# Optimization experiments

Hardware: AMD Instinct MI355X
Metric: run time of the kernel (lower is better)

## Reference

```python
import jax, jax.numpy as jnp
import numpy as np

MARGIN = 0.3
MIN_POS_DIST = 0.1
PUSH_SCALE = 2.0
DISSIMILAR_REL = 1  # dissimilar_relation_ids == {1}


def setup_inputs() -> dict:
    key = jax.random.key(0)
    k1, k2, k3, k4, k5 = jax.random.split(key, 5)
    B, D = 16384, 1024
    h = jax.random.normal(k1, (B, D), dtype=jnp.float32)
    t = jax.random.normal(k2, (B, D), dtype=jnp.float32)
    r = jax.random.normal(k3, (B, D), dtype=jnp.float32)
    relation_ids = jax.random.randint(k4, (B,), 0, 10, dtype=jnp.int64 if jax.config.jax_enable_x64 else jnp.int32)
    neg = jax.random.randint(k5, (B,), 0, B, dtype=relation_ids.dtype)
    idx = jnp.arange(B, dtype=neg.dtype)
    neg_idx = jnp.where(neg == idx, (neg + 1) % B, neg)  # enforce neg_idx[i] != i
    return {"h": h, "t": t, "r": r, "relation_ids": relation_ids, "neg_idx": neg_idx}


def reference(h, t, r, relation_ids, neg_idx):
    # pos_dist[i] = ||h[i] + r[i] - t[i]||_2
    hr = h + r                                  # [B, D]
    pos_dist = jnp.linalg.norm(hr - t, axis=-1)  # [B]
    # neg_dist[i] = ||h[i] + r[i] - t[neg_idx[i]]||_2
    neg_dist = jnp.linalg.norm(hr - t[neg_idx], axis=-1)  # [B]

    dissim = relation_ids == DISSIMILAR_REL
    curr_margin = MARGIN * PUSH_SCALE
    loss_dissim = jax.nn.relu(curr_margin - pos_dist) + 0.5 * jnp.exp(-pos_dist)
    loss_sim = jax.nn.relu(pos_dist - neg_dist + MARGIN) + 0.3 * jax.nn.relu(MIN_POS_DIST - pos_dist)
    per_sample = jnp.where(dissim, loss_dissim, loss_sim)
    return jnp.mean(per_sample)
```

## Files before the change

### kernel.cpp

```cpp
#include <hip/hip_runtime.h>
#include <math.h>


#define BDIM 16384
#define DDIM 1024
#define NBLK (BDIM / 4)

typedef float vfloat4 __attribute__((ext_vector_type(4)));

__global__ void zero_out_kernel(float* __restrict__ out) { out[0] = 0.0f; }

template <int USE_WS>
__global__ __launch_bounds__(256, 4) void triplet_partial_kernel(
    const float* __restrict__ h, const float* __restrict__ t,
    const float* __restrict__ r, const int* __restrict__ rel,
    const int* __restrict__ neg, float* __restrict__ sink)
{
    __shared__ float sm[4];

    const int wave = threadIdx.x >> 6;
    const int lane = threadIdx.x & 63;
    const int row  = (blockIdx.x << 2) + wave;

    const int nidx = neg[row];
    const int rl   = rel[row];

    const vfloat4* hb = (const vfloat4*)(h + (size_t)row * DDIM) + lane;
    const vfloat4* rb = (const vfloat4*)(r + (size_t)row * DDIM) + lane;
    const vfloat4* tb = (const vfloat4*)(t + (size_t)row * DDIM) + lane;
    const vfloat4* nb = (rl == 1) ? tb
                       : (const vfloat4*)(t + (size_t)nidx * DDIM) + lane;

    vfloat4 hv[4], rv[4], tv[4], nv[4];
#pragma unroll
    for (int c = 0; c < 4; ++c) {
        hv[c] = hb[c << 6];
        rv[c] = rb[c << 6];
        tv[c] = tb[c << 6];
        nv[c] = nb[c << 6];
    }
    __builtin_amdgcn_sched_barrier(0);

    float psum = 0.0f, nsum = 0.0f;
#pragma unroll
    for (int c = 0; c < 4; ++c) {
        vfloat4 a = hv[c] + rv[c];
        vfloat4 d = a - tv[c];
        vfloat4 e = a - nv[c];
        psum += d.x * d.x + d.y * d.y + d.z * d.z + d.w * d.w;
        nsum += e.x * e.x + e.y * e.y + e.z * e.z + e.w * e.w;
    }

#pragma unroll
    for (int off = 32; off > 0; off >>= 1) {
        psum += __shfl_down(psum, off, 64);
        nsum += __shfl_down(nsum, off, 64);
    }

    if (lane == 0) {
        float pos  = sqrtf(psum);
        float negd = sqrtf(nsum);
        float loss;
        if (rl == 1) loss = fmaxf(0.6f - pos, 0.0f) + 0.5f * expf(-pos);
        else         loss = fmaxf(pos - negd + 0.3f, 0.0f)
                          + 0.3f * fmaxf(0.1f - pos, 0.0f);
        sm[wave] = loss;
    }
    __syncthreads();
    if (threadIdx.x == 0) {
        float blk = sm[0] + sm[1] + sm[2] + sm[3];
        if (USE_WS) {
            sink[blockIdx.x] = blk;
        } else {
            atomicAdd(sink, blk * (1.0f / (float)BDIM));
        }
    }
}

__global__ __launch_bounds__(1024) void reduce_partials_kernel(
    const float* __restrict__ ws, float* __restrict__ out)
{
    __shared__ float sm[16];
    const int tid  = threadIdx.x;
    const int wave = tid >> 6;
    const int lane = tid & 63;

    vfloat4 v = ((const vfloat4*)ws)[tid];
    float s = v.x + v.y + v.z + v.w;

#pragma unroll
    for (int off = 32; off > 0; off >>= 1)
        s += __shfl_down(s, off, 64);

    if (lane == 0) sm[wave] = s;
    __syncthreads();
    if (tid == 0) {
        float tot = 0.0f;
#pragma unroll
        for (int w = 0; w < 16; ++w) tot += sm[w];
        out[0] = tot * (1.0f / (float)BDIM);
    }
}

extern "C" void kernel_launch(void* const* d_in, const int* in_sizes, int n_in,
                              void* d_out, int out_size, void* d_ws, size_t ws_size,
                              hipStream_t stream) {
    const float* h = (const float*)d_in[0];
    const float* t = (const float*)d_in[1];
    const float* r = (const float*)d_in[2];
    const int* rel = (const int*)d_in[3];
    const int* neg = (const int*)d_in[4];
    float* out = (float*)d_out;
    float* ws  = (float*)d_ws;

    if (ws != nullptr && ws_size >= NBLK * sizeof(float)) {
        triplet_partial_kernel<1><<<NBLK, 256, 0, stream>>>(h, t, r, rel, neg, ws);
        reduce_partials_kernel<<<1, 1024, 0, stream>>>(ws, out);
    } else {
        zero_out_kernel<<<1, 1, 0, stream>>>(out);
        triplet_partial_kernel<0><<<NBLK, 256, 0, stream>>>(h, t, r, rel, neg, out);
    }
}
```

Before: 202.4 us.

## Process four rows per wave to cut block count and amortize reductions

Each wave now computes four rows instead of one, loading relation and negative indices as int4 vectors and reducing four partial sums per shuffle pass. The grid shrinks by four and the final reduce kernel is resized to 256 threads. This is meant to amortize per-block launch, index-load and reduction overhead, at the cost of fewer waves in flight and higher register pressure if all row loads are hoisted together.

Result: no change. 202.6 us (+0.1%).

```diff
diff --git a/kernel.cpp b/kernel.cpp
--- a/kernel.cpp
+++ b/kernel.cpp
@@ -4,9 +4,10 @@
 
 #define BDIM 16384
 #define DDIM 1024
-#define NBLK (BDIM / 4)
+#define NBLK (BDIM / 16)
 
 typedef float vfloat4 __attribute__((ext_vector_type(4)));
+typedef int   vint4   __attribute__((ext_vector_type(4)));
 
 __global__ void zero_out_kernel(float* __restrict__ out) { out[0] = 0.0f; }
 
@@ -20,51 +21,66 @@
 
     const int wave = threadIdx.x >> 6;
     const int lane = threadIdx.x & 63;
-    const int row  = (blockIdx.x << 2) + wave;
+    const int r0   = ((blockIdx.x << 2) + wave) << 2;
 
-    const int nidx = neg[row];
-    const int rl   = rel[row];
+    const vint4 nidx = *(const vint4*)(neg + r0);
+    const vint4 rli  = *(const vint4*)(rel + r0);
 
-    const vfloat4* hb = (const vfloat4*)(h + (size_t)row * DDIM) + lane;
-    const vfloat4* rb = (const vfloat4*)(r + (size_t)row * DDIM) + lane;
-    const vfloat4* tb = (const vfloat4*)(t + (size_t)row * DDIM) + lane;
-    const vfloat4* nb = (rl == 1) ? tb
-                       : (const vfloat4*)(t + (size_t)nidx * DDIM) + lane;
+    float psum[4], nsum[4];
+    float loss[4];
 
-    vfloat4 hv[4], rv[4], tv[4], nv[4];
 #pragma unroll
-    for (int c = 0; c < 4; ++c) {
-        hv[c] = hb[c << 6];
-        rv[c] = rb[c << 6];
-        tv[c] = tb[c << 6];
-        nv[c] = nb[c << 6];
-    }
-    __builtin_amdgcn_sched_barrier(0);
+    for (int j = 0; j < 4; ++j) {
+        const int row = r0 + j;
+        const vfloat4* hb = (const vfloat4*)(h + (size_t)row * DDIM) + lane;
+        const vfloat4* rb = (const vfloat4*)(r + (size_t)row * DDIM) + lane;
+        const vfloat4* tb = (const vfloat4*)(t + (size_t)row * DDIM) + lane;
+        const vfloat4* nb = (rli[j] == 1) ? tb
+                           : (const vfloat4*)(t + (size_t)nidx[j] * DDIM) + lane;
 
-    float psum = 0.0f, nsum = 0.0f;
+        vfloat4 hv[4], rv[4], tv[4], nv[4];
 #pragma unroll
-    for (int c = 0; c < 4; ++c) {
-        vfloat4 a = hv[c] + rv[c];
-        vfloat4 d = a - tv[c];
-        vfloat4 e = a - nv[c];
-        psum += d.x * d.x + d.y * d.y + d.z * d.z + d.w * d.w;
-        nsum += e.x * e.x + e.y * e.y + e.z * e.z + e.w * e.w;
+        for (int c = 0; c < 4; ++c) {
+            hv[c] = hb[c << 6];
+            rv[c] = rb[c << 6];
+            tv[c] = tb[c << 6];
+            nv[c] = nb[c << 6];
+        }
+
+        float ps = 0.0f, ns = 0.0f;
+#pragma unroll
+        for (int c = 0; c < 4; ++c) {
+            vfloat4 a = hv[c] + rv[c];
+            vfloat4 d = a - tv[c];
+            vfloat4 e = a - nv[c];
+            ps += d.x * d.x + d.y * d.y + d.z * d.z + d.w * d.w;
+            ns += e.x * e.x + e.y * e.y + e.z * e.z + e.w * e.w;
+        }
+        psum[j] = ps;
+        nsum[j] = ns;
     }
 
 #pragma unroll
     for (int off = 32; off > 0; off >>= 1) {
-        psum += __shfl_down(psum, off, 64);
-        nsum += __shfl_down(nsum, off, 64);
+#pragma unroll
+        for (int j = 0; j < 4; ++j) {
+            psum[j] += __shfl_down(psum[j], off, 64);
+            nsum[j] += __shfl_down(nsum[j], off, 64);
+        }
     }
 
     if (lane == 0) {
-        float pos  = sqrtf(psum);
-        float negd = sqrtf(nsum);
-        float loss;
-        if (rl == 1) loss = fmaxf(0.6f - pos, 0.0f) + 0.5f * expf(-pos);
-        else         loss = fmaxf(pos - negd + 0.3f, 0.0f)
-                          + 0.3f * fmaxf(0.1f - pos, 0.0f);
-        sm[wave] = loss;
+#pragma unroll
+        for (int j = 0; j < 4; ++j) {
+            float pos  = sqrtf(psum[j]);
+            float negd = sqrtf(nsum[j]);
+            if (rli[j] == 1)
+                loss[j] = fmaxf(0.6f - pos, 0.0f) + 0.5f * expf(-pos);
+            else
+                loss[j] = fmaxf(pos - negd + 0.3f, 0.0f)
+                        + 0.3f * fmaxf(0.1f - pos, 0.0f);
+        }
+        sm[wave] = loss[0] + loss[1] + loss[2] + loss[3];
     }
     __syncthreads();
     if (threadIdx.x == 0) {
@@ -77,10 +93,10 @@
     }
 }
 
-__global__ __launch_bounds__(1024) void reduce_partials_kernel(
+__global__ __launch_bounds__(256) void reduce_partials_kernel(
     const float* __restrict__ ws, float* __restrict__ out)
 {
-    __shared__ float sm[16];
+    __shared__ float sm[4];
     const int tid  = threadIdx.x;
     const int wave = tid >> 6;
     const int lane = tid & 63;
@@ -94,12 +110,8 @@
 
     if (lane == 0) sm[wave] = s;
     __syncthreads();
-    if (tid == 0) {
-        float tot = 0.0f;
-#pragma unroll
-        for (int w = 0; w < 16; ++w) tot += sm[w];
-        out[0] = tot * (1.0f / (float)BDIM);
-    }
+    if (tid == 0)
+        out[0] = (sm[0] + sm[1] + sm[2] + sm[3]) * (1.0f / (float)BDIM);
 }
 
 extern "C" void kernel_launch(void* const* d_in, const int* in_sizes, int n_in,
@@ -115,7 +127,7 @@
 
     if (ws != nullptr && ws_size >= NBLK * sizeof(float)) {
         triplet_partial_kernel<1><<<NBLK, 256, 0, stream>>>(h, t, r, rel, neg, ws);
-        reduce_partials_kernel<<<1, 1024, 0, stream>>>(ws, out);
+        reduce_partials_kernel<<<1, 256, 0, stream>>>(ws, out);
     } else {
         zero_out_kernel<<<1, 1, 0, stream>>>(out);
         triplet_partial_kernel<0><<<NBLK, 256, 0, stream>>>(h, t, r, rel, neg, out);
```
